# Optimization experiments

Measured on AMD Instinct MI355X. Metric: run time of the kernel, lower is better.

The kernel has to match this reference:

```python
import jax, jax.numpy as jnp
import numpy as np

N_NODES = 50000


def setup_inputs() -> dict:
    key = jax.random.key(0)
    k1, k2, k3, k4, k5 = jax.random.split(key, 5)
    N, E, D, U = N_NODES, 1600000, 128, 128
    node_features = jax.random.normal(k1, (N, D), dtype=jnp.float32)
    edge_src = jax.random.randint(k2, (E,), 0, N, dtype=jnp.int32)
    edge_dst = jax.random.randint(k3, (E,), 0, N, dtype=jnp.int32)
    edge_weight = jax.random.uniform(k4, (E,), dtype=jnp.float32)
    W = jax.random.normal(k5, (D, U), dtype=jnp.float32) * (1.0 / np.sqrt(D))
    b = jnp.zeros((U,), dtype=jnp.float32)
    return {"node_features": node_features, "edge_src": edge_src,
            "edge_dst": edge_dst, "edge_weight": edge_weight, "W": W, "b": b}


def reference(node_features, edge_src, edge_dst, edge_weight, W, b):
    # embedding_lookup_sparse_v2(..., combiner='mean'):
    #   agg[i] = sum_{e: src[e]=i} w[e] * feat[dst[e]] / sum_{e: src[e]=i} w[e]
    gathered = node_features[edge_dst] * edge_weight[:, None]        # [E, D]
    num = jax.ops.segment_sum(gathered, edge_src, num_segments=N_NODES)   # [N, D]
    den = jax.ops.segment_sum(edge_weight, edge_src, num_segments=N_NODES)  # [N]
    agg = num / jnp.maximum(den, 1e-12)[:, None]
    # Dense(units, activation='relu'); dropout is identity at inference
    return jax.nn.relu(agg @ W + b)
```

## Files before the change

### kernel.cpp

```cpp
#include <hip/hip_runtime.h>
#include <hip/hip_bf16.h>


typedef unsigned int vuint4 __attribute__((ext_vector_type(4)));
typedef short bf16x8 __attribute__((ext_vector_type(8)));
typedef float f32x4 __attribute__((ext_vector_type(4)));
typedef float f32x2 __attribute__((ext_vector_type(2)));

#define SRCSH 8
#define BNODES 256
#define BCAP 9728
#define PCAP 11776
#define NBLK 512
#define AGG_NBLK 2048

__device__ __forceinline__ unsigned short f2bf(float f) {
    unsigned u = __float_as_uint(f);
    unsigned r = (u + 0x7fff + ((u >> 16) & 1)) >> 16;
    return (unsigned short)r;
}
__device__ __forceinline__ float bf2f(unsigned short h) {
    return __uint_as_float(((unsigned)h) << 16);
}

__global__ __launch_bounds__(256)
void histA_kernel(const float* __restrict__ feat, ushort* __restrict__ featb,
                  const float* __restrict__ W, ushort* __restrict__ WT,
                  const int* __restrict__ esrc, int* __restrict__ cnt,
                  int E, int nbuk, int N, int D) {
    __shared__ int hcnt[256];
    int tid = threadIdx.x, blk = blockIdx.x;

    {
        int gid = blk * 256 + tid;
        int gstr = NBLK * 256;
        int nf4 = N * D / 4;
        for (int i = gid; i < nf4; i += gstr) {
            float4 v = ((const float4*)feat)[i];
            ushort4 r;
            r.x = f2bf(v.x); r.y = f2bf(v.y); r.z = f2bf(v.z); r.w = f2bf(v.w);
            ((ushort4*)featb)[i] = r;
        }
        int nw = D * D;
        for (int i = gid; i < nw; i += gstr) {
            int u = i >> 7, k = i & 127;
            WT[i] = f2bf(W[k * 128 + u]);
        }
    }

    hcnt[tid] = 0;
    __syncthreads();

    int per = ((E + NBLK - 1) / NBLK + 3) & ~3;
    int lo = blk * per;
    int hi = lo + per; if (hi > E) hi = E;
    for (int i4 = (lo >> 2) + tid; i4 < (hi >> 2); i4 += 256) {
        int4 s = ((const int4*)esrc)[i4];
        atomicAdd(&hcnt[s.x >> SRCSH], 1);
        atomicAdd(&hcnt[s.y >> SRCSH], 1);
        atomicAdd(&hcnt[s.z >> SRCSH], 1);
        atomicAdd(&hcnt[s.w >> SRCSH], 1);
    }
    __syncthreads();
    if (tid < nbuk) cnt[blk * nbuk + tid] = hcnt[tid];
}

__global__ __launch_bounds__(256)
void scanB_kernel(const int* __restrict__ cnt, int* __restrict__ hbase,
                  int* __restrict__ gtot, int nbuk) {
    int lane = threadIdx.x & 63, wid = threadIdx.x >> 6;
    int b = blockIdx.x * 4 + wid;
    if (b >= nbuk) return;

    int v[8]; int run = 0;
    #pragma unroll
    for (int i = 0; i < 8; ++i) {
        v[i] = cnt[(lane * 8 + i) * nbuk + b];
        run += v[i];
    }
    int x = run;
    #pragma unroll
    for (int off = 1; off < 64; off <<= 1) {
        int y = __shfl_up(x, off, 64);
        if (lane >= off) x += y;
    }
    int excl = x - run;
    #pragma unroll
    for (int i = 0; i < 8; ++i) {
        hbase[b * NBLK + lane * 8 + i] = excl;
        excl += v[i];
    }
    if (lane == 63) gtot[b] = x;
}

__global__ __launch_bounds__(256)
void scatterC_kernel(const int* __restrict__ esrc, const int* __restrict__ edst,
                     const float* __restrict__ ew, const int* __restrict__ hbase,
                     unsigned long long* __restrict__ staging, int E, int nbuk) {
    __shared__ int hb[256];
    __shared__ int hoff[256];
    int tid = threadIdx.x, blk = blockIdx.x;
    if (tid < nbuk) { hb[tid] = hbase[tid * NBLK + blk]; }
    hoff[tid] = 0;
    __syncthreads();

    int per = ((E + NBLK - 1) / NBLK + 3) & ~3;
    int lo = blk * per;
    int hi = lo + per; if (hi > E) hi = E;
    for (int i4 = (lo >> 2) + tid; i4 < (hi >> 2); i4 += 256) {
        int4 s = ((const int4*)esrc)[i4];
        int4 d = ((const int4*)edst)[i4];
        float4 w = ((const float4*)ew)[i4];
        #pragma unroll
        for (int k = 0; k < 4; ++k) {
            int sv = (k == 0) ? s.x : (k == 1) ? s.y : (k == 2) ? s.z : s.w;
            int dv = (k == 0) ? d.x : (k == 1) ? d.y : (k == 2) ? d.z : d.w;
            float wv = (k == 0) ? w.x : (k == 1) ? w.y : (k == 2) ? w.z : w.w;
            int b = sv >> SRCSH;
            int pos = hb[b] + atomicAdd(&hoff[b], 1);
            if (pos < BCAP) {
                unsigned long long v = ((unsigned long long)__float_as_uint(wv) << 32)
                                     | ((unsigned long long)(sv & (BNODES - 1)) << 16)
                                     | (unsigned long long)(unsigned)dv;
                staging[(size_t)b * BCAP + pos] = v;
            }
        }
    }
}

__global__ __launch_bounds__(256)
void finB_kernel(const int* __restrict__ gtot, const unsigned long long* __restrict__ staging,
                 unsigned* __restrict__ pay4, int* __restrict__ rs, int* __restrict__ re, int N) {
    __shared__ int hist[BNODES];
    __shared__ int hcur[BNODES];
    __shared__ int ws[4];
    int b = blockIdx.x, tid = threadIdx.x;
    hist[tid] = 0;
    __syncthreads();

    int m = gtot[b]; if (m > BCAP) m = BCAP;
    size_t sbase = (size_t)b * BCAP;
    for (int i = tid; i < m; i += 256) {
        unsigned long long v = staging[sbase + i];
        atomicAdd(&hist[(int)((v >> 16) & (BNODES - 1))], 1);
    }
    __syncthreads();

    int lane = tid & 63, wid = tid >> 6;
    int h = hist[tid];
    int p = (h + 7) & ~7;
    int x = p;
    #pragma unroll
    for (int off = 1; off < 64; off <<= 1) {
        int y = __shfl_up(x, off, 64);
        if (lane >= off) x += y;
    }
    if (lane == 63) ws[wid] = x;
    __syncthreads();
    if (tid == 0) { int a = 0; for (int w = 0; w < 4; ++w) { int t = ws[w]; ws[w] = a; a += t; } }
    __syncthreads();
    int excl = ws[wid] + x - p;

    int gb = b * PCAP;
    hcur[tid] = excl;
    int n = b * BNODES + tid;
    if (n < N) { rs[n] = gb + excl; re[n] = gb + excl + p; }
    for (int i = excl + h; i < excl + p; ++i) pay4[gb + i] = 0;
    __syncthreads();

    for (int i = tid; i < m; i += 256) {
        unsigned long long v = staging[sbase + i];
        int s8 = (int)((v >> 16) & (BNODES - 1));
        int pos = atomicAdd(&hcur[s8], 1);
        unsigned wbf = f2bf(__uint_as_float((unsigned)(v >> 32)));
        pay4[gb + pos] = (wbf << 16) | (unsigned)(v & 0xffffu);
    }
}

__global__ __launch_bounds__(256, 8)
void agg_kernel(const ushort* __restrict__ featb, const unsigned* __restrict__ pay4,
                const int* __restrict__ rs, const int* __restrict__ re,
                ushort* __restrict__ aggb, int N) {
    int tid = threadIdx.x, lane = tid & 63, wid = tid >> 6;
    const ushort2* feat2 = (const ushort2*)featb;
    ushort2* agg2 = (ushort2*)aggb;

    const int NW = AGG_NBLK * 4;
    for (int n = blockIdx.x * 4 + wid; n < N; n += NW) {
        int p = rs[n], pend = re[n];
        f32x2 axy = (f32x2){0.f, 0.f};
        float wsum = 0.f;

        if (p < pend) {
            vuint4 qa = __builtin_nontemporal_load((const vuint4*)(pay4 + p));
            vuint4 qb = __builtin_nontemporal_load((const vuint4*)(pay4 + p + 4));
            while (p < pend) {
                p += 8;
                vuint4 na, nb;
                bool more = p < pend;
                if (more) {
                    na = __builtin_nontemporal_load((const vuint4*)(pay4 + p));
                    nb = __builtin_nontemporal_load((const vuint4*)(pay4 + p + 4));
                }
                unsigned q[8] = {qa.x, qa.y, qa.z, qa.w, qb.x, qb.y, qb.z, qb.w};
                unsigned fu[8];
                #pragma unroll
                for (int k = 0; k < 8; ++k)
                    fu[k] = *(const unsigned*)&feat2[(q[k] & 0xffffu) * 64 + lane];
                #pragma unroll
                for (int k = 0; k < 8; ++k) {
                    float w = __uint_as_float(q[k] & 0xffff0000u);
                    f32x2 f;
                    f.x = __uint_as_float(fu[k] << 16);
                    f.y = __uint_as_float(fu[k] & 0xffff0000u);
                    axy += w * f;
                    wsum += w;
                }
                qa = na; qb = nb;
            }
        }
        float inv = 1.f / fmaxf(wsum, 1e-12f);
        ushort2 o;
        o.x = f2bf(axy.x * inv);
        o.y = f2bf(axy.y * inv);
        agg2[(size_t)n * 64 + lane] = o;
    }
}

__global__ __launch_bounds__(256)
void gemm_kernel(const ushort* __restrict__ aggb, const ushort* __restrict__ WT,
                 const float* __restrict__ bias, float* __restrict__ out, int ntiles) {
    int tid = threadIdx.x, lane = tid & 63, wid = tid >> 6;
    int tile = blockIdx.x * 4 + wid;
    if (tile >= ntiles) return;
    int m = lane & 15, quad = lane >> 4;

    f32x4 acc[8];
    #pragma unroll
    for (int t = 0; t < 8; ++t) acc[t] = (f32x4){0.f, 0.f, 0.f, 0.f};

    #pragma unroll
    for (int ks = 0; ks < 4; ++ks) {
        bf16x8 a = *(const bf16x8*)(aggb + ((size_t)(tile * 16 + m) * 128 + ks * 32 + quad * 8));
        #pragma unroll
        for (int nt = 0; nt < 8; ++nt) {
            bf16x8 bfr = *(const bf16x8*)(WT + ((nt * 16 + m) * 128 + ks * 32 + quad * 8));
            acc[nt] = __builtin_amdgcn_mfma_f32_16x16x32_bf16(a, bfr, acc[nt], 0, 0, 0);
        }
    }

    #pragma unroll
    for (int nt = 0; nt < 8; ++nt) {
        int col = nt * 16 + m;
        float bv = bias[col];
        #pragma unroll
        for (int r = 0; r < 4; ++r) {
            int row = tile * 16 + quad * 4 + r;
            float v = fmaxf(acc[nt][r] + bv, 0.f);
            __builtin_nontemporal_store(v, out + (size_t)row * 128 + col);
        }
    }
}

extern "C" void kernel_launch(void* const* d_in, const int* in_sizes, int n_in,
                              void* d_out, int out_size, void* d_ws, size_t ws_size,
                              hipStream_t stream) {
    const float* feat = (const float*)d_in[0];
    const int*   esrc = (const int*)d_in[1];
    const int*   edst = (const int*)d_in[2];
    const float* ew   = (const float*)d_in[3];
    const float* W    = (const float*)d_in[4];
    const float* bias = (const float*)d_in[5];
    float* out = (float*)d_out;

    const int D = 128;
    int N = in_sizes[0] / D;
    int E = in_sizes[1];
    int nbuk = (N + BNODES - 1) >> SRCSH;

    unsigned long long* staging = (unsigned long long*)d_ws;
    int* cnt   = (int*)(staging + (size_t)nbuk * BCAP);
    int* hbase = cnt + (size_t)NBLK * nbuk;
    int* gtot  = hbase + (size_t)nbuk * NBLK;
    int* rs    = gtot + nbuk;
    int* re    = rs + N;
    unsigned* pay4 = (unsigned*)(re + N);
    ushort* featb = (ushort*)(pay4 + (size_t)nbuk * PCAP);
    ushort* aggb  = featb + (size_t)N * D;
    ushort* WT    = aggb + (size_t)N * D;

    histA_kernel<<<NBLK, 256, 0, stream>>>(feat, featb, W, WT, esrc, cnt, E, nbuk, N, D);
    scanB_kernel<<<(nbuk + 3) / 4, 256, 0, stream>>>(cnt, hbase, gtot, nbuk);
    scatterC_kernel<<<NBLK, 256, 0, stream>>>(esrc, edst, ew, hbase, staging, E, nbuk);
    finB_kernel<<<nbuk, 256, 0, stream>>>(gtot, staging, pay4, rs, re, N);
    agg_kernel<<<AGG_NBLK, 256, 0, stream>>>(featb, pay4, rs, re, aggb, N);
    int ntiles = N / 16;
    gemm_kernel<<<(ntiles + 3) / 4, 256, 0, stream>>>(aggb, WT, bias, out, ntiles);
}
```

Before: 226.5 us.

## Fuse six pipeline kernels into one cooperative persistent kernel with grid syncs

Merges the histogram, scan, scatter, bucket-finalize, aggregation and GEMM kernels into a single cooperative kernel. Grid-wide barriers separate the phases, and each phase loops over its work items with a grid-stride loop. The aim is to remove five kernel launch gaps and tail effects. In exchange, every phase is limited to the occupancy the fused kernel's register use allows. The aggregation loses its separate launch bounds of 8 blocks per CU, and each grid.sync adds its own cost.

Result: slower. 495.5 us (+118.7%).

```diff
diff --git a/kernel.cpp b/kernel.cpp
--- a/kernel.cpp
+++ b/kernel.cpp
@@ -1,6 +1,9 @@
 #include <hip/hip_runtime.h>
 #include <hip/hip_bf16.h>
-
+#include <hip/hip_cooperative_groups.h>
+
+
+namespace cg = cooperative_groups;
 
 typedef unsigned int vuint4 __attribute__((ext_vector_type(4)));
 typedef short bf16x8 __attribute__((ext_vector_type(8)));
@@ -12,7 +15,7 @@
 #define BCAP 9728
 #define PCAP 11776
 #define NBLK 512
-#define AGG_NBLK 2048
+#define MAXG 2048
 
 __device__ __forceinline__ unsigned short f2bf(float f) {
     unsigned u = __float_as_uint(f);
@@ -24,240 +27,223 @@
 }
 
 __global__ __launch_bounds__(256)
-void histA_kernel(const float* __restrict__ feat, ushort* __restrict__ featb,
-                  const float* __restrict__ W, ushort* __restrict__ WT,
-                  const int* __restrict__ esrc, int* __restrict__ cnt,
-                  int E, int nbuk, int N, int D) {
-    __shared__ int hcnt[256];
-    int tid = threadIdx.x, blk = blockIdx.x;
+void fused_kernel(const float* __restrict__ feat, const int* __restrict__ esrc,
+                  const int* __restrict__ edst, const float* __restrict__ ew,
+                  const float* __restrict__ W, const float* __restrict__ bias,
+                  float* __restrict__ out,
+                  unsigned long long* __restrict__ staging, int* __restrict__ cnt,
+                  int* __restrict__ hbase, int* __restrict__ gtot,
+                  int* __restrict__ rs, int* __restrict__ re,
+                  unsigned* __restrict__ pay4, ushort* __restrict__ featb,
+                  ushort* __restrict__ aggb, ushort* __restrict__ WT,
+                  int E, int nbuk, int N) {
+    cg::grid_group grid = cg::this_grid();
+    __shared__ int sh_a[256];
+    __shared__ int sh_b[256];
+    __shared__ int sh_ws[4];
+    int tid = threadIdx.x, lane = tid & 63, wid = tid >> 6;
+    int gblk = blockIdx.x, G = gridDim.x;
+    int per = ((E + NBLK - 1) / NBLK + 3) & ~3;
 
     {
-        int gid = blk * 256 + tid;
-        int gstr = NBLK * 256;
-        int nf4 = N * D / 4;
+        int gid = gblk * 256 + tid, gstr = G * 256;
+        int nf4 = N * 128 / 4;
         for (int i = gid; i < nf4; i += gstr) {
             float4 v = ((const float4*)feat)[i];
             ushort4 r;
             r.x = f2bf(v.x); r.y = f2bf(v.y); r.z = f2bf(v.z); r.w = f2bf(v.w);
             ((ushort4*)featb)[i] = r;
         }
-        int nw = D * D;
-        for (int i = gid; i < nw; i += gstr) {
+        for (int i = gid; i < 128 * 128; i += gstr) {
             int u = i >> 7, k = i & 127;
             WT[i] = f2bf(W[k * 128 + u]);
         }
     }
 
-    hcnt[tid] = 0;
-    __syncthreads();
-
-    int per = ((E + NBLK - 1) / NBLK + 3) & ~3;
-    int lo = blk * per;
-    int hi = lo + per; if (hi > E) hi = E;
-    for (int i4 = (lo >> 2) + tid; i4 < (hi >> 2); i4 += 256) {
-        int4 s = ((const int4*)esrc)[i4];
-        atomicAdd(&hcnt[s.x >> SRCSH], 1);
-        atomicAdd(&hcnt[s.y >> SRCSH], 1);
-        atomicAdd(&hcnt[s.z >> SRCSH], 1);
-        atomicAdd(&hcnt[s.w >> SRCSH], 1);
-    }
-    __syncthreads();
-    if (tid < nbuk) cnt[blk * nbuk + tid] = hcnt[tid];
-}
-
-__global__ __launch_bounds__(256)
-void scanB_kernel(const int* __restrict__ cnt, int* __restrict__ hbase,
-                  int* __restrict__ gtot, int nbuk) {
-    int lane = threadIdx.x & 63, wid = threadIdx.x >> 6;
-    int b = blockIdx.x * 4 + wid;
-    if (b >= nbuk) return;
-
-    int v[8]; int run = 0;
-    #pragma unroll
-    for (int i = 0; i < 8; ++i) {
-        v[i] = cnt[(lane * 8 + i) * nbuk + b];
-        run += v[i];
-    }
-    int x = run;
-    #pragma unroll
-    for (int off = 1; off < 64; off <<= 1) {
-        int y = __shfl_up(x, off, 64);
-        if (lane >= off) x += y;
-    }
-    int excl = x - run;
-    #pragma unroll
-    for (int i = 0; i < 8; ++i) {
-        hbase[b * NBLK + lane * 8 + i] = excl;
-        excl += v[i];
-    }
-    if (lane == 63) gtot[b] = x;
-}
-
-__global__ __launch_bounds__(256)
-void scatterC_kernel(const int* __restrict__ esrc, const int* __restrict__ edst,
-                     const float* __restrict__ ew, const int* __restrict__ hbase,
-                     unsigned long long* __restrict__ staging, int E, int nbuk) {
-    __shared__ int hb[256];
-    __shared__ int hoff[256];
-    int tid = threadIdx.x, blk = blockIdx.x;
-    if (tid < nbuk) { hb[tid] = hbase[tid * NBLK + blk]; }
-    hoff[tid] = 0;
-    __syncthreads();
-
-    int per = ((E + NBLK - 1) / NBLK + 3) & ~3;
-    int lo = blk * per;
-    int hi = lo + per; if (hi > E) hi = E;
-    for (int i4 = (lo >> 2) + tid; i4 < (hi >> 2); i4 += 256) {
-        int4 s = ((const int4*)esrc)[i4];
-        int4 d = ((const int4*)edst)[i4];
-        float4 w = ((const float4*)ew)[i4];
-        #pragma unroll
-        for (int k = 0; k < 4; ++k) {
-            int sv = (k == 0) ? s.x : (k == 1) ? s.y : (k == 2) ? s.z : s.w;
-            int dv = (k == 0) ? d.x : (k == 1) ? d.y : (k == 2) ? d.z : d.w;
-            float wv = (k == 0) ? w.x : (k == 1) ? w.y : (k == 2) ? w.z : w.w;
-            int b = sv >> SRCSH;
-            int pos = hb[b] + atomicAdd(&hoff[b], 1);
-            if (pos < BCAP) {
-                unsigned long long v = ((unsigned long long)__float_as_uint(wv) << 32)
-                                     | ((unsigned long long)(sv & (BNODES - 1)) << 16)
-                                     | (unsigned long long)(unsigned)dv;
-                staging[(size_t)b * BCAP + pos] = v;
-            }
-        }
-    }
-}
-
-__global__ __launch_bounds__(256)
-void finB_kernel(const int* __restrict__ gtot, const unsigned long long* __restrict__ staging,
-                 unsigned* __restrict__ pay4, int* __restrict__ rs, int* __restrict__ re, int N) {
-    __shared__ int hist[BNODES];
-    __shared__ int hcur[BNODES];
-    __shared__ int ws[4];
-    int b = blockIdx.x, tid = threadIdx.x;
-    hist[tid] = 0;
-    __syncthreads();
-
-    int m = gtot[b]; if (m > BCAP) m = BCAP;
-    size_t sbase = (size_t)b * BCAP;
-    for (int i = tid; i < m; i += 256) {
-        unsigned long long v = staging[sbase + i];
-        atomicAdd(&hist[(int)((v >> 16) & (BNODES - 1))], 1);
-    }
-    __syncthreads();
-
-    int lane = tid & 63, wid = tid >> 6;
-    int h = hist[tid];
-    int p = (h + 7) & ~7;
-    int x = p;
-    #pragma unroll
-    for (int off = 1; off < 64; off <<= 1) {
-        int y = __shfl_up(x, off, 64);
-        if (lane >= off) x += y;
-    }
-    if (lane == 63) ws[wid] = x;
-    __syncthreads();
-    if (tid == 0) { int a = 0; for (int w = 0; w < 4; ++w) { int t = ws[w]; ws[w] = a; a += t; } }
-    __syncthreads();
-    int excl = ws[wid] + x - p;
-
-    int gb = b * PCAP;
-    hcur[tid] = excl;
-    int n = b * BNODES + tid;
-    if (n < N) { rs[n] = gb + excl; re[n] = gb + excl + p; }
-    for (int i = excl + h; i < excl + p; ++i) pay4[gb + i] = 0;
-    __syncthreads();
-
-    for (int i = tid; i < m; i += 256) {
-        unsigned long long v = staging[sbase + i];
-        int s8 = (int)((v >> 16) & (BNODES - 1));
-        int pos = atomicAdd(&hcur[s8], 1);
-        unsigned wbf = f2bf(__uint_as_float((unsigned)(v >> 32)));
-        pay4[gb + pos] = (wbf << 16) | (unsigned)(v & 0xffffu);
-    }
-}
-
-__global__ __launch_bounds__(256, 8)
-void agg_kernel(const ushort* __restrict__ featb, const unsigned* __restrict__ pay4,
-                const int* __restrict__ rs, const int* __restrict__ re,
-                ushort* __restrict__ aggb, int N) {
-    int tid = threadIdx.x, lane = tid & 63, wid = tid >> 6;
-    const ushort2* feat2 = (const ushort2*)featb;
-    ushort2* agg2 = (ushort2*)aggb;
-
-    const int NW = AGG_NBLK * 4;
-    for (int n = blockIdx.x * 4 + wid; n < N; n += NW) {
-        int p = rs[n], pend = re[n];
-        f32x2 axy = (f32x2){0.f, 0.f};
-        float wsum = 0.f;
-
-        if (p < pend) {
-            vuint4 qa = __builtin_nontemporal_load((const vuint4*)(pay4 + p));
-            vuint4 qb = __builtin_nontemporal_load((const vuint4*)(pay4 + p + 4));
-            while (p < pend) {
-                p += 8;
-                vuint4 na, nb;
-                bool more = p < pend;
-                if (more) {
-                    na = __builtin_nontemporal_load((const vuint4*)(pay4 + p));
-                    nb = __builtin_nontemporal_load((const vuint4*)(pay4 + p + 4));
-                }
-                unsigned q[8] = {qa.x, qa.y, qa.z, qa.w, qb.x, qb.y, qb.z, qb.w};
-                unsigned fu[8];
+    for (int blk = gblk; blk < NBLK; blk += G) {
+        sh_a[tid] = 0;
+        __syncthreads();
+        int lo = blk * per, hi = lo + per; if (hi > E) hi = E;
+        for (int i4 = (lo >> 2) + tid; i4 < (hi >> 2); i4 += 256) {
+            int4 s = ((const int4*)esrc)[i4];
+            atomicAdd(&sh_a[s.x >> SRCSH], 1);
+            atomicAdd(&sh_a[s.y >> SRCSH], 1);
+            atomicAdd(&sh_a[s.z >> SRCSH], 1);
+            atomicAdd(&sh_a[s.w >> SRCSH], 1);
+        }
+        __syncthreads();
+        if (tid < nbuk) cnt[blk * nbuk + tid] = sh_a[tid];
+        __syncthreads();
+    }
+    grid.sync();
+
+    for (int b = gblk * 4 + wid; b < nbuk; b += G * 4) {
+        int v[8]; int run = 0;
+        #pragma unroll
+        for (int i = 0; i < 8; ++i) {
+            v[i] = cnt[(lane * 8 + i) * nbuk + b];
+            run += v[i];
+        }
+        int x = run;
+        #pragma unroll
+        for (int off = 1; off < 64; off <<= 1) {
+            int y = __shfl_up(x, off, 64);
+            if (lane >= off) x += y;
+        }
+        int excl = x - run;
+        #pragma unroll
+        for (int i = 0; i < 8; ++i) {
+            hbase[b * NBLK + lane * 8 + i] = excl;
+            excl += v[i];
+        }
+        if (lane == 63) gtot[b] = x;
+    }
+    grid.sync();
+
+    for (int blk = gblk; blk < NBLK; blk += G) {
+        if (tid < nbuk) sh_a[tid] = hbase[tid * NBLK + blk];
+        sh_b[tid] = 0;
+        __syncthreads();
+        int lo = blk * per, hi = lo + per; if (hi > E) hi = E;
+        for (int i4 = (lo >> 2) + tid; i4 < (hi >> 2); i4 += 256) {
+            int4 s = ((const int4*)esrc)[i4];
+            int4 d = ((const int4*)edst)[i4];
+            float4 w = ((const float4*)ew)[i4];
+            #pragma unroll
+            for (int k = 0; k < 4; ++k) {
+                int sv = (k == 0) ? s.x : (k == 1) ? s.y : (k == 2) ? s.z : s.w;
+                int dv = (k == 0) ? d.x : (k == 1) ? d.y : (k == 2) ? d.z : d.w;
+                float wv = (k == 0) ? w.x : (k == 1) ? w.y : (k == 2) ? w.z : w.w;
+                int b = sv >> SRCSH;
+                int pos = sh_a[b] + atomicAdd(&sh_b[b], 1);
+                if (pos < BCAP) {
+                    unsigned long long v = ((unsigned long long)__float_as_uint(wv) << 32)
+                                         | ((unsigned long long)(sv & (BNODES - 1)) << 16)
+                                         | (unsigned long long)(unsigned)(dv & 0xffff);
+                    staging[(size_t)b * BCAP + pos] = v;
+                }
+            }
+        }
+        __syncthreads();
+    }
+    grid.sync();
+
+    for (int b = gblk; b < nbuk; b += G) {
+        sh_a[tid] = 0;
+        __syncthreads();
+
+        int m = gtot[b]; if (m > BCAP) m = BCAP;
+        size_t sbase = (size_t)b * BCAP;
+        for (int i = tid; i < m; i += 256) {
+            unsigned long long v = staging[sbase + i];
+            atomicAdd(&sh_a[(int)((v >> 16) & (BNODES - 1))], 1);
+        }
+        __syncthreads();
+
+        int h = sh_a[tid];
+        int p = (h + 7) & ~7;
+        int x = p;
+        #pragma unroll
+        for (int off = 1; off < 64; off <<= 1) {
+            int y = __shfl_up(x, off, 64);
+            if (lane >= off) x += y;
+        }
+        if (lane == 63) sh_ws[wid] = x;
+        __syncthreads();
+        if (tid == 0) { int a = 0; for (int w = 0; w < 4; ++w) { int t = sh_ws[w]; sh_ws[w] = a; a += t; } }
+        __syncthreads();
+        int excl = sh_ws[wid] + x - p;
+
+        int gb = b * PCAP;
+        sh_b[tid] = excl;
+        int n = b * BNODES + tid;
+        if (n < N) { rs[n] = gb + excl; re[n] = gb + excl + p; }
+        for (int i = excl + h; i < excl + p; ++i) pay4[gb + i] = 0;
+        __syncthreads();
+
+        for (int i = tid; i < m; i += 256) {
+            unsigned long long v = staging[sbase + i];
+            int s8 = (int)((v >> 16) & (BNODES - 1));
+            int pos = atomicAdd(&sh_b[s8], 1);
+            unsigned wbf = f2bf(__uint_as_float((unsigned)(v >> 32)));
+            pay4[gb + pos] = (wbf << 16) | (unsigned)(v & 0xffffu);
+        }
+        __syncthreads();
+    }
+    grid.sync();
+
+    {
+        const ushort2* feat2 = (const ushort2*)featb;
+        ushort2* agg2 = (ushort2*)aggb;
+        int NW = G * 4;
+        for (int n = gblk * 4 + wid; n < N; n += NW) {
+            int pp = rs[n], pend = re[n];
+            f32x2 axy = (f32x2){0.f, 0.f};
+            float wsum = 0.f;
+            if (pp < pend) {
+                vuint4 qa = __builtin_nontemporal_load((const vuint4*)(pay4 + pp));
+                vuint4 qb = __builtin_nontemporal_load((const vuint4*)(pay4 + pp + 4));
+                while (pp < pend) {
+                    pp += 8;
+                    vuint4 na, nb;
+                    bool more = pp < pend;
+                    if (more) {
+                        na = __builtin_nontemporal_load((const vuint4*)(pay4 + pp));
+                        nb = __builtin_nontemporal_load((const vuint4*)(pay4 + pp + 4));
+                    }
+                    unsigned q[8] = {qa.x, qa.y, qa.z, qa.w, qb.x, qb.y, qb.z, qb.w};
+                    unsigned fu[8];
+                    #pragma unroll
+                    for (int k = 0; k < 8; ++k)
+                        fu[k] = *(const unsigned*)&feat2[(q[k] & 0xffffu) * 64 + lane];
+                    #pragma unroll
+                    for (int k = 0; k < 8; ++k) {
+                        float w = __uint_as_float(q[k] & 0xffff0000u);
+                        f32x2 f;
+                        f.x = __uint_as_float(fu[k] << 16);
+                        f.y = __uint_as_float(fu[k] & 0xffff0000u);
+                        axy += w * f;
+                        wsum += w;
+                    }
+                    qa = na; qb = nb;
+                }
+            }
+            float inv = 1.f / fmaxf(wsum, 1e-12f);
+            ushort2 o;
+            o.x = f2bf(axy.x * inv);
+            o.y = f2bf(axy.y * inv);
+            agg2[(size_t)n * 64 + lane] = o;
+        }
+    }
+    grid.sync();
+
+    {
+        int ntiles = N / 16;
+        int m = lane & 15, quad = lane >> 4;
+        for (int tile = gblk * 4 + wid; tile < ntiles; tile += G * 4) {
+            f32x4 acc[8];
+            #pragma unroll
+            for (int t = 0; t < 8; ++t) acc[t] = (f32x4){0.f, 0.f, 0.f, 0.f};
+            #pragma unroll
+            for (int ks = 0; ks < 4; ++ks) {
+                bf16x8 a = *(const bf16x8*)(aggb + ((size_t)(tile * 16 + m) * 128 + ks * 32 + quad * 8));
                 #pragma unroll
-                for (int k = 0; k < 8; ++k)
-                    fu[k] = *(const unsigned*)&feat2[(q[k] & 0xffffu) * 64 + lane];
+                for (int nt = 0; nt < 8; ++nt) {
+                    bf16x8 bfr = *(const bf16x8*)(WT + (nt * 16 + m) * 128 + ks * 32 + quad * 8);
+                    acc[nt] = __builtin_amdgcn_mfma_f32_16x16x32_bf16(a, bfr, acc[nt], 0, 0, 0);
+                }
+            }
+            #pragma unroll
+            for (int nt = 0; nt < 8; ++nt) {
+                int col = nt * 16 + m;
+                float bv = bias[col];
                 #pragma unroll
-                for (int k = 0; k < 8; ++k) {
-                    float w = __uint_as_float(q[k] & 0xffff0000u);
-                    f32x2 f;
-                    f.x = __uint_as_float(fu[k] << 16);
-                    f.y = __uint_as_float(fu[k] & 0xffff0000u);
-                    axy += w * f;
-                    wsum += w;
-                }
-                qa = na; qb = nb;
-            }
-        }
-        float inv = 1.f / fmaxf(wsum, 1e-12f);
-        ushort2 o;
-        o.x = f2bf(axy.x * inv);
-        o.y = f2bf(axy.y * inv);
-        agg2[(size_t)n * 64 + lane] = o;
-    }
-}
-
-__global__ __launch_bounds__(256)
-void gemm_kernel(const ushort* __restrict__ aggb, const ushort* __restrict__ WT,
-                 const float* __restrict__ bias, float* __restrict__ out, int ntiles) {
-    int tid = threadIdx.x, lane = tid & 63, wid = tid >> 6;
-    int tile = blockIdx.x * 4 + wid;
-    if (tile >= ntiles) return;
-    int m = lane & 15, quad = lane >> 4;
-
-    f32x4 acc[8];
-    #pragma unroll
-    for (int t = 0; t < 8; ++t) acc[t] = (f32x4){0.f, 0.f, 0.f, 0.f};
-
-    #pragma unroll
-    for (int ks = 0; ks < 4; ++ks) {
-        bf16x8 a = *(const bf16x8*)(aggb + ((size_t)(tile * 16 + m) * 128 + ks * 32 + quad * 8));
-        #pragma unroll
-        for (int nt = 0; nt < 8; ++nt) {
-            bf16x8 bfr = *(const bf16x8*)(WT + ((nt * 16 + m) * 128 + ks * 32 + quad * 8));
-            acc[nt] = __builtin_amdgcn_mfma_f32_16x16x32_bf16(a, bfr, acc[nt], 0, 0, 0);
-        }
-    }
-
-    #pragma unroll
-    for (int nt = 0; nt < 8; ++nt) {
-        int col = nt * 16 + m;
-        float bv = bias[col];
-        #pragma unroll
-        for (int r = 0; r < 4; ++r) {
-            int row = tile * 16 + quad * 4 + r;
-            float v = fmaxf(acc[nt][r] + bv, 0.f);
-            __builtin_nontemporal_store(v, out + (size_t)row * 128 + col);
+                for (int r = 0; r < 4; ++r) {
+                    int row = tile * 16 + quad * 4 + r;
+                    float v = fmaxf(acc[nt][r] + bv, 0.f);
+                    __builtin_nontemporal_store(v, out + (size_t)row * 128 + col);
+                }
+            }
         }
     }
 }
@@ -289,11 +275,21 @@
     ushort* aggb  = featb + (size_t)N * D;
     ushort* WT    = aggb + (size_t)N * D;
 
-    histA_kernel<<<NBLK, 256, 0, stream>>>(feat, featb, W, WT, esrc, cnt, E, nbuk, N, D);
-    scanB_kernel<<<(nbuk + 3) / 4, 256, 0, stream>>>(cnt, hbase, gtot, nbuk);
-    scatterC_kernel<<<NBLK, 256, 0, stream>>>(esrc, edst, ew, hbase, staging, E, nbuk);
-    finB_kernel<<<nbuk, 256, 0, stream>>>(gtot, staging, pay4, rs, re, N);
-    agg_kernel<<<AGG_NBLK, 256, 0, stream>>>(featb, pay4, rs, re, aggb, N);
-    int ntiles = N / 16;
-    gemm_kernel<<<(ntiles + 3) / 4, 256, 0, stream>>>(aggb, WT, bias, out, ntiles);
-}
+    static int gridBlocks = 0;
+    if (gridBlocks == 0) {
+        int perCU = 0, cus = 0;
+        hipOccupancyMaxActiveBlocksPerMultiprocessor(&perCU, (const void*)fused_kernel, 256, 0);
+        hipDeviceGetAttribute(&cus, hipDeviceAttributeMultiprocessorCount, 0);
+        if (perCU < 1) perCU = 1;
+        if (cus < 1) cus = 256;
+        gridBlocks = perCU * cus;
+        if (gridBlocks > MAXG) gridBlocks = MAXG;
+    }
+
+    void* args[] = {(void*)&feat, (void*)&esrc, (void*)&edst, (void*)&ew, (void*)&W,
+                    (void*)&bias, (void*)&out, (void*)&staging, (void*)&cnt, (void*)&hbase,
+                    (void*)&gtot, (void*)&rs, (void*)&re, (void*)&pay4, (void*)&featb,
+                    (void*)&aggb, (void*)&WT, (void*)&E, (void*)&nbuk, (void*)&N};
+    hipLaunchCooperativeKernel((const void*)fused_kernel, dim3(gridBlocks), dim3(256),
+                               args, 0, stream);
+}
```

## Fuse histogram/scan/scatter into one kernel and quarter-split edges by destination for locality

Applied to the files above, without the earlier changes.

The separate histogram, scan and scatter kernels are merged into one kernel that reserves per-bucket ranges with global atomics, removing two launches and the count/base arrays. The finalize pass now sorts each source node's edges into four sub-ranges keyed by destination-id quarter. The aggregation kernel processes 13 nodes per wave and walks quarter by quarter, so feature gathers in flight at once hit a smaller slice of the feature table and get better cache reuse. In exchange, edge order within a bucket becomes nondeterministic, there is more padding, and the aggregation carries more register state per wave. The aggregation output now reuses the staging buffer.

Result: slower. 277.2 us (+22.4%).

```diff
diff --git a/kernel.cpp b/kernel.cpp
--- a/kernel.cpp
+++ b/kernel.cpp
@@ -10,9 +10,13 @@
 #define SRCSH 8
 #define BNODES 256
 #define BCAP 9728
-#define PCAP 11776
+#define NQ 4
+#define QSH 14
+#define NKEY 1024
+#define PCAP 14336
 #define NBLK 512
-#define AGG_NBLK 2048
+#define AGG_BLOCKS 1024
+#define CNT 13
 
 __device__ __forceinline__ unsigned short f2bf(float f) {
     unsigned u = __float_as_uint(f);
@@ -24,16 +28,18 @@
 }
 
 __global__ __launch_bounds__(256)
-void histA_kernel(const float* __restrict__ feat, ushort* __restrict__ featb,
+void sortA_kernel(const float* __restrict__ feat, ushort* __restrict__ featb,
                   const float* __restrict__ W, ushort* __restrict__ WT,
-                  const int* __restrict__ esrc, int* __restrict__ cnt,
+                  const int* __restrict__ esrc, const int* __restrict__ edst,
+                  const float* __restrict__ ew, int* __restrict__ gcur,
+                  unsigned long long* __restrict__ staging,
                   int E, int nbuk, int N, int D) {
     __shared__ int hcnt[256];
+    __shared__ int base[256];
     int tid = threadIdx.x, blk = blockIdx.x;
 
     {
-        int gid = blk * 256 + tid;
-        int gstr = NBLK * 256;
+        int gid = blk * 256 + tid, gstr = NBLK * 256;
         int nf4 = N * D / 4;
         for (int i = gid; i < nf4; i += gstr) {
             float4 v = ((const float4*)feat)[i];
@@ -41,8 +47,7 @@
             r.x = f2bf(v.x); r.y = f2bf(v.y); r.z = f2bf(v.z); r.w = f2bf(v.w);
             ((ushort4*)featb)[i] = r;
         }
-        int nw = D * D;
-        for (int i = gid; i < nw; i += gstr) {
+        for (int i = gid; i < D * D; i += gstr) {
             int u = i >> 7, k = i & 127;
             WT[i] = f2bf(W[k * 128 + u]);
         }
@@ -54,6 +59,7 @@
     int per = ((E + NBLK - 1) / NBLK + 3) & ~3;
     int lo = blk * per;
     int hi = lo + per; if (hi > E) hi = E;
+
     for (int i4 = (lo >> 2) + tid; i4 < (hi >> 2); i4 += 256) {
         int4 s = ((const int4*)esrc)[i4];
         atomicAdd(&hcnt[s.x >> SRCSH], 1);
@@ -62,51 +68,12 @@
         atomicAdd(&hcnt[s.w >> SRCSH], 1);
     }
     __syncthreads();
-    if (tid < nbuk) cnt[blk * nbuk + tid] = hcnt[tid];
-}
-
-__global__ __launch_bounds__(256)
-void scanB_kernel(const int* __restrict__ cnt, int* __restrict__ hbase,
-                  int* __restrict__ gtot, int nbuk) {
-    int lane = threadIdx.x & 63, wid = threadIdx.x >> 6;
-    int b = blockIdx.x * 4 + wid;
-    if (b >= nbuk) return;
-
-    int v[8]; int run = 0;
-    #pragma unroll
-    for (int i = 0; i < 8; ++i) {
-        v[i] = cnt[(lane * 8 + i) * nbuk + b];
-        run += v[i];
-    }
-    int x = run;
-    #pragma unroll
-    for (int off = 1; off < 64; off <<= 1) {
-        int y = __shfl_up(x, off, 64);
-        if (lane >= off) x += y;
-    }
-    int excl = x - run;
-    #pragma unroll
-    for (int i = 0; i < 8; ++i) {
-        hbase[b * NBLK + lane * 8 + i] = excl;
-        excl += v[i];
-    }
-    if (lane == 63) gtot[b] = x;
-}
-
-__global__ __launch_bounds__(256)
-void scatterC_kernel(const int* __restrict__ esrc, const int* __restrict__ edst,
-                     const float* __restrict__ ew, const int* __restrict__ hbase,
-                     unsigned long long* __restrict__ staging, int E, int nbuk) {
-    __shared__ int hb[256];
-    __shared__ int hoff[256];
-    int tid = threadIdx.x, blk = blockIdx.x;
-    if (tid < nbuk) { hb[tid] = hbase[tid * NBLK + blk]; }
-    hoff[tid] = 0;
-    __syncthreads();
-
-    int per = ((E + NBLK - 1) / NBLK + 3) & ~3;
-    int lo = blk * per;
-    int hi = lo + per; if (hi > E) hi = E;
+
+    if (tid < nbuk) base[tid] = atomicAdd(&gcur[tid], hcnt[tid]);
+    __syncthreads();
+    hcnt[tid] = 0;
+    __syncthreads();
+
     for (int i4 = (lo >> 2) + tid; i4 < (hi >> 2); i4 += 256) {
         int4 s = ((const int4*)esrc)[i4];
         int4 d = ((const int4*)edst)[i4];
@@ -117,11 +84,11 @@
             int dv = (k == 0) ? d.x : (k == 1) ? d.y : (k == 2) ? d.z : d.w;
             float wv = (k == 0) ? w.x : (k == 1) ? w.y : (k == 2) ? w.z : w.w;
             int b = sv >> SRCSH;
-            int pos = hb[b] + atomicAdd(&hoff[b], 1);
+            int pos = base[b] + atomicAdd(&hcnt[b], 1);
             if (pos < BCAP) {
                 unsigned long long v = ((unsigned long long)__float_as_uint(wv) << 32)
                                      | ((unsigned long long)(sv & (BNODES - 1)) << 16)
-                                     | (unsigned long long)(unsigned)dv;
+                                     | (unsigned long long)(unsigned)(dv & 0xffff);
                 staging[(size_t)b * BCAP + pos] = v;
             }
         }
@@ -129,101 +96,133 @@
 }
 
 __global__ __launch_bounds__(256)
-void finB_kernel(const int* __restrict__ gtot, const unsigned long long* __restrict__ staging,
-                 unsigned* __restrict__ pay4, int* __restrict__ rs, int* __restrict__ re, int N) {
-    __shared__ int hist[BNODES];
-    __shared__ int hcur[BNODES];
-    __shared__ int ws[4];
-    int b = blockIdx.x, tid = threadIdx.x;
-    hist[tid] = 0;
+void finq_kernel(const int* __restrict__ gtot, const unsigned long long* __restrict__ staging,
+                 unsigned* __restrict__ pay4, int4* __restrict__ rs4, int* __restrict__ re,
+                 int N) {
+    __shared__ int hist[NKEY];
+    __shared__ int cur[NKEY];
+    __shared__ int ws4[4];
+    int b = blockIdx.x, tid = threadIdx.x, lane = tid & 63, wid = tid >> 6;
+
+    for (int i = tid; i < NKEY; i += 256) hist[i] = 0;
     __syncthreads();
 
     int m = gtot[b]; if (m > BCAP) m = BCAP;
     size_t sbase = (size_t)b * BCAP;
     for (int i = tid; i < m; i += 256) {
         unsigned long long v = staging[sbase + i];
-        atomicAdd(&hist[(int)((v >> 16) & (BNODES - 1))], 1);
-    }
-    __syncthreads();
-
-    int lane = tid & 63, wid = tid >> 6;
-    int h = hist[tid];
-    int p = (h + 7) & ~7;
-    int x = p;
+        int key = ((int)((v >> 16) & 255)) * 4 + (int)((v & 0xffffu) >> QSH);
+        atomicAdd(&hist[key], 1);
+    }
+    __syncthreads();
+
+    int h0 = hist[4 * tid], h1 = hist[4 * tid + 1], h2 = hist[4 * tid + 2], h3 = hist[4 * tid + 3];
+    int p0 = (h0 + 7) & ~7, p1 = (h1 + 7) & ~7, p2 = (h2 + 7) & ~7, p3 = (h3 + 7) & ~7;
+    int s = p0 + p1 + p2 + p3;
+    int x = s;
     #pragma unroll
     for (int off = 1; off < 64; off <<= 1) {
         int y = __shfl_up(x, off, 64);
         if (lane >= off) x += y;
     }
-    if (lane == 63) ws[wid] = x;
-    __syncthreads();
-    if (tid == 0) { int a = 0; for (int w = 0; w < 4; ++w) { int t = ws[w]; ws[w] = a; a += t; } }
-    __syncthreads();
-    int excl = ws[wid] + x - p;
-
+    if (lane == 63) ws4[wid] = x;
+    __syncthreads();
+    if (tid == 0) { int a = 0; for (int w = 0; w < 4; ++w) { int t = ws4[w]; ws4[w] = a; a += t; } }
+    __syncthreads();
+    int excl = ws4[wid] + x - s;
+
+    int e0 = excl, e1 = e0 + p0, e2 = e1 + p1, e3 = e2 + p2;
     int gb = b * PCAP;
-    hcur[tid] = excl;
+    cur[4 * tid] = e0; cur[4 * tid + 1] = e1; cur[4 * tid + 2] = e2; cur[4 * tid + 3] = e3;
     int n = b * BNODES + tid;
-    if (n < N) { rs[n] = gb + excl; re[n] = gb + excl + p; }
-    for (int i = excl + h; i < excl + p; ++i) pay4[gb + i] = 0;
+    if (n < N) {
+        rs4[n] = make_int4(gb + e0, gb + e1, gb + e2, gb + e3);
+        re[n] = gb + e3 + p3;
+    }
+    for (int i = e0 + h0; i < e0 + p0; ++i) if (i < PCAP) pay4[gb + i] = 0;
+    for (int i = e1 + h1; i < e1 + p1; ++i) if (i < PCAP) pay4[gb + i] = 0;
+    for (int i = e2 + h2; i < e2 + p2; ++i) if (i < PCAP) pay4[gb + i] = 0;
+    for (int i = e3 + h3; i < e3 + p3; ++i) if (i < PCAP) pay4[gb + i] = 0;
     __syncthreads();
 
     for (int i = tid; i < m; i += 256) {
         unsigned long long v = staging[sbase + i];
-        int s8 = (int)((v >> 16) & (BNODES - 1));
-        int pos = atomicAdd(&hcur[s8], 1);
+        int key = ((int)((v >> 16) & 255)) * 4 + (int)((v & 0xffffu) >> QSH);
+        int pos = atomicAdd(&cur[key], 1);
         unsigned wbf = f2bf(__uint_as_float((unsigned)(v >> 32)));
-        pay4[gb + pos] = (wbf << 16) | (unsigned)(v & 0xffffu);
-    }
-}
-
-__global__ __launch_bounds__(256, 8)
+        if (pos < PCAP) pay4[gb + pos] = (wbf << 16) | (unsigned)(v & 0xffffu);
+    }
+}
+
+__global__ __launch_bounds__(256)
 void agg_kernel(const ushort* __restrict__ featb, const unsigned* __restrict__ pay4,
-                const int* __restrict__ rs, const int* __restrict__ re,
+                const int* __restrict__ rs4i, const int* __restrict__ re,
                 ushort* __restrict__ aggb, int N) {
     int tid = threadIdx.x, lane = tid & 63, wid = tid >> 6;
     const ushort2* feat2 = (const ushort2*)featb;
     ushort2* agg2 = (ushort2*)aggb;
-
-    const int NW = AGG_NBLK * 4;
-    for (int n = blockIdx.x * 4 + wid; n < N; n += NW) {
-        int p = rs[n], pend = re[n];
-        f32x2 axy = (f32x2){0.f, 0.f};
-        float wsum = 0.f;
-
-        if (p < pend) {
-            vuint4 qa = __builtin_nontemporal_load((const vuint4*)(pay4 + p));
-            vuint4 qb = __builtin_nontemporal_load((const vuint4*)(pay4 + p + 4));
-            while (p < pend) {
-                p += 8;
-                vuint4 na, nb;
-                bool more = p < pend;
-                if (more) {
-                    na = __builtin_nontemporal_load((const vuint4*)(pay4 + p));
-                    nb = __builtin_nontemporal_load((const vuint4*)(pay4 + p + 4));
+    int gw = blockIdx.x * 4 + wid;
+    const int NW = AGG_BLOCKS * 4;
+
+    f32x2 axy[CNT];
+    float wsum[CNT];
+    #pragma unroll
+    for (int i = 0; i < CNT; ++i) { axy[i] = (f32x2){0.f, 0.f}; wsum[i] = 0.f; }
+
+    for (int q = 0; q < NQ; ++q) {
+        int pB[CNT], pE[CNT];
+        #pragma unroll
+        for (int i = 0; i < CNT; ++i) {
+            int n = gw + i * NW;
+            if (n < N) {
+                pB[i] = rs4i[n * 4 + q];
+                pE[i] = (q < 3) ? rs4i[n * 4 + q + 1] : re[n];
+            } else { pB[i] = 0; pE[i] = 0; }
+        }
+        #pragma unroll
+        for (int i = 0; i < CNT; ++i) {
+            int p = pB[i], pend = pE[i];
+            if (p < pend) {
+                vuint4 qa = __builtin_nontemporal_load((const vuint4*)(pay4 + p));
+                vuint4 qb = __builtin_nontemporal_load((const vuint4*)(pay4 + p + 4));
+                while (p < pend) {
+                    p += 8;
+                    vuint4 na, nb;
+                    bool more = p < pend;
+                    if (more) {
+                        na = __builtin_nontemporal_load((const vuint4*)(pay4 + p));
+                        nb = __builtin_nontemporal_load((const vuint4*)(pay4 + p + 4));
+                    }
+                    unsigned qv[8] = {qa.x, qa.y, qa.z, qa.w, qb.x, qb.y, qb.z, qb.w};
+                    unsigned fu[8];
+                    #pragma unroll
+                    for (int k = 0; k < 8; ++k)
+                        fu[k] = *(const unsigned*)&feat2[(qv[k] & 0xffffu) * 64 + lane];
+                    #pragma unroll
+                    for (int k = 0; k < 8; ++k) {
+                        float w = __uint_as_float(qv[k] & 0xffff0000u);
+                        f32x2 f;
+                        f.x = __uint_as_float(fu[k] << 16);
+                        f.y = __uint_as_float(fu[k] & 0xffff0000u);
+                        axy[i] += w * f;
+                        wsum[i] += w;
+                    }
+                    qa = na; qb = nb;
                 }
-                unsigned q[8] = {qa.x, qa.y, qa.z, qa.w, qb.x, qb.y, qb.z, qb.w};
-                unsigned fu[8];
-                #pragma unroll
-                for (int k = 0; k < 8; ++k)
-                    fu[k] = *(const unsigned*)&feat2[(q[k] & 0xffffu) * 64 + lane];
-                #pragma unroll
-                for (int k = 0; k < 8; ++k) {
-                    float w = __uint_as_float(q[k] & 0xffff0000u);
-                    f32x2 f;
-                    f.x = __uint_as_float(fu[k] << 16);
-                    f.y = __uint_as_float(fu[k] & 0xffff0000u);
-                    axy += w * f;
-                    wsum += w;
-                }
-                qa = na; qb = nb;
             }
         }
-        float inv = 1.f / fmaxf(wsum, 1e-12f);
-        ushort2 o;
-        o.x = f2bf(axy.x * inv);
-        o.y = f2bf(axy.y * inv);
-        agg2[(size_t)n * 64 + lane] = o;
+    }
+
+    #pragma unroll
+    for (int i = 0; i < CNT; ++i) {
+        int n = gw + i * NW;
+        if (n < N) {
+            float inv = 1.f / fmaxf(wsum[i], 1e-12f);
+            ushort2 o;
+            o.x = f2bf(axy[i].x * inv);
+            o.y = f2bf(axy[i].y * inv);
+            agg2[(size_t)n * 64 + lane] = o;
+        }
     }
 }
 
@@ -279,21 +278,19 @@
     int nbuk = (N + BNODES - 1) >> SRCSH;
 
     unsigned long long* staging = (unsigned long long*)d_ws;
-    int* cnt   = (int*)(staging + (size_t)nbuk * BCAP);
-    int* hbase = cnt + (size_t)NBLK * nbuk;
-    int* gtot  = hbase + (size_t)nbuk * NBLK;
-    int* rs    = gtot + nbuk;
-    int* re    = rs + N;
-    unsigned* pay4 = (unsigned*)(re + N);
-    ushort* featb = (ushort*)(pay4 + (size_t)nbuk * PCAP);
-    ushort* aggb  = featb + (size_t)N * D;
-    ushort* WT    = aggb + (size_t)N * D;
-
-    histA_kernel<<<NBLK, 256, 0, stream>>>(feat, featb, W, WT, esrc, cnt, E, nbuk, N, D);
-    scanB_kernel<<<(nbuk + 3) / 4, 256, 0, stream>>>(cnt, hbase, gtot, nbuk);
-    scatterC_kernel<<<NBLK, 256, 0, stream>>>(esrc, edst, ew, hbase, staging, E, nbuk);
-    finB_kernel<<<nbuk, 256, 0, stream>>>(gtot, staging, pay4, rs, re, N);
-    agg_kernel<<<AGG_NBLK, 256, 0, stream>>>(featb, pay4, rs, re, aggb, N);
+    unsigned* pay4 = (unsigned*)(staging + (size_t)nbuk * BCAP);
+    int* rs4i = (int*)(pay4 + (size_t)nbuk * PCAP);
+    int* re   = rs4i + (size_t)4 * N;
+    int* gcur = re + N;
+    ushort* featb = (ushort*)(gcur + 256);
+    ushort* WT    = featb + (size_t)N * D;
+    ushort* aggb  = (ushort*)staging;
+
+    hipMemsetAsync(gcur, 0, 256 * sizeof(int), stream);
+    sortA_kernel<<<NBLK, 256, 0, stream>>>(feat, featb, W, WT, esrc, edst, ew,
+                                           gcur, staging, E, nbuk, N, D);
+    finq_kernel<<<nbuk, 256, 0, stream>>>(gcur, staging, pay4, (int4*)rs4i, re, N);
+    agg_kernel<<<AGG_BLOCKS, 256, 0, stream>>>(featb, pay4, rs4i, re, aggb, N);
     int ntiles = N / 16;
     gemm_kernel<<<(ntiles + 3) / 4, 256, 0, stream>>>(aggb, WT, bias, out, ntiles);
 }
```
